# Performance work log

Measured on AMD Instinct MI355X. Metric: run time of the kernel, lower is better.

Reference implementation:

```python
import jax, jax.numpy as jnp
import numpy as np

HEADS = 16
DIM_HEAD = 64
DIM = 1024
INNER = HEADS * DIM_HEAD


def setup_inputs() -> dict:
    key = jax.random.key(0)
    k1, k2, k3, k4 = jax.random.split(key, 4)
    x = jax.random.normal(k1, (4, 2048, DIM), dtype=jnp.float32)
    W_qkv = jax.random.normal(k2, (DIM, 3 * INNER), dtype=jnp.float32) * (DIM ** -0.5)
    W_out = jax.random.normal(k3, (INNER, DIM), dtype=jnp.float32) * (INNER ** -0.5)
    b_out = jax.random.normal(k4, (DIM,), dtype=jnp.float32) * 0.01
    temperature = jnp.asarray(np.log(DIM_HEAD ** -0.5), dtype=jnp.float32)
    return {"x": x, "W_qkv": W_qkv, "W_out": W_out, "b_out": b_out,
            "temperature": temperature}


def reference(x, W_qkv, W_out, b_out, temperature):
    b, n, _ = x.shape
    qkv = jnp.einsum('bnd,de->bne', x, W_qkv)  # [b, n, 3*inner]
    q, k, v = jnp.split(qkv, 3, axis=-1)
    def split_heads(t):
        return t.reshape(b, n, HEADS, DIM_HEAD).transpose(0, 2, 1, 3)  # b h n d
    q, k, v = split_heads(q), split_heads(k), split_heads(v)
    scale = jnp.exp(temperature)
    dots = jnp.einsum('bhid,bhjd->bhij', q, k) * scale  # [b, h, n, n]
    mask_value = -jnp.finfo(dots.dtype).max
    eye = jnp.eye(n, dtype=bool)
    dots = jnp.where(eye, mask_value, dots)
    attn = jax.nn.softmax(dots, axis=-1)
    out = jnp.einsum('bhij,bhjd->bhid', attn, v)  # [b, h, n, d]
    out = out.transpose(0, 2, 1, 3).reshape(b, n, INNER)
    return jnp.einsum('bni,id->bnd', out, W_out) + b_out
```

## Files before the change

kernel.cpp:

```cpp
#include <hip/hip_runtime.h>


using u16 = unsigned short;
typedef short short8 __attribute__((ext_vector_type(8)));
typedef float floatx4 __attribute__((ext_vector_type(4)));
typedef float floatx16 __attribute__((ext_vector_type(16)));
typedef unsigned int uint2v __attribute__((ext_vector_type(2)));

#define B_ 4
#define N_ 2048
#define H_ 16
#define DH_ 64
#define D_ 1024
#define INNER_ 1024
#define M_ (B_ * N_)

__device__ __forceinline__ float bf2f(u16 h) {
    union { unsigned u; float f; } c; c.u = ((unsigned)h) << 16; return c.f;
}
__device__ __forceinline__ u16 f2bf(float f) {
    union { float f; unsigned u; } c; c.f = f;
    unsigned u = c.u + 0x7fffu + ((c.u >> 16) & 1u);
    return (u16)(u >> 16);
}
__device__ __forceinline__ unsigned cvtpk_bf16(float lo, float hi) {
    unsigned r;
    asm("v_cvt_pk_bf16_f32 %0, %1, %2" : "=v"(r) : "v"(lo), "v"(hi));
    return r;
}
__device__ __forceinline__ float fast_exp2(float x) {
#if defined(__has_builtin) && __has_builtin(__builtin_amdgcn_exp2f)
    return __builtin_amdgcn_exp2f(x);
#else
    return __expf(x * 0.69314718056f);
#endif
}
__device__ __forceinline__ void gl2lds16(const u16* g, u16* l) {
    __builtin_amdgcn_global_load_lds(
        (const __attribute__((address_space(1))) void*)g,
        (__attribute__((address_space(3))) void*)l, 16, 0, 0);
}

__global__ void detect_dtype(const u16* __restrict__ x, int* __restrict__ flag) {
    __shared__ int cnt;
    if (threadIdx.x == 0) cnt = 0;
    __syncthreads();
    int c = 0;
    for (int i = threadIdx.x; i < 4096; i += 256) {
        int e = (x[i] >> 7) & 0xFF;
        if (e >= 107 && e <= 147) c++;
    }
    atomicAdd(&cnt, c);
    __syncthreads();
    if (threadIdx.x == 0) flag[0] = (cnt >= 3584) ? 1 : 0;
}

__global__ __launch_bounds__(256) void convert_x(
    const void* __restrict__ in, u16* __restrict__ out, int n,
    const int* __restrict__ flag) {
    int f = flag[0];
    int i0 = (blockIdx.x * 256 + threadIdx.x) * 8;
    if (f) {
        const u16* p = (const u16*)in;
        for (int i = 0; i < 8; i++) out[i0 + i] = p[i0 + i];
    } else {
        const float* p = (const float*)in;
        for (int i = 0; i < 8; i++) out[i0 + i] = f2bf(p[i0 + i]);
    }
}

__global__ void prep_misc(const void* __restrict__ bias_in,
                          const void* __restrict__ temp_in,
                          float* __restrict__ bias_f, float* __restrict__ temp_f,
                          const int* __restrict__ flag) {
    int f = flag[0];
    for (int i = threadIdx.x; i < 1024; i += 256)
        bias_f[i] = f ? bf2f(((const u16*)bias_in)[i]) : ((const float*)bias_in)[i];
    if (threadIdx.x == 0)
        temp_f[0] = f ? bf2f(((const u16*)temp_in)[0]) : ((const float*)temp_in)[0];
}

__global__ __launch_bounds__(256) void transpose_cvt(
    const void* __restrict__ in, u16* __restrict__ out, int R, int C,
    const int* __restrict__ flag) {
    __shared__ u16 t[32][33];
    int f = flag[0];
    int tx = threadIdx.x & 31, ty = threadIdx.x >> 5;
    int c0 = blockIdx.x * 32, r0 = blockIdx.y * 32;
    for (int i = 0; i < 4; i++) {
        long idx = (long)(r0 + ty + i * 8) * C + c0 + tx;
        t[ty + i * 8][tx] = f ? ((const u16*)in)[idx] : f2bf(((const float*)in)[idx]);
    }
    __syncthreads();
    for (int i = 0; i < 4; i++)
        out[(long)(c0 + ty + i * 8) * R + r0 + tx] = t[tx][ty + i * 8];
}

__global__ __launch_bounds__(256) void transpose_v(
    const u16* __restrict__ in, u16* __restrict__ out) {
    __shared__ u16 t[32][33];
    const int bh = blockIdx.z;
    const u16* src = in + (long)bh * N_ * DH_;
    u16* dst = out + (long)bh * DH_ * N_;
    int tx = threadIdx.x & 31, ty = threadIdx.x >> 5;
    int r0 = blockIdx.y * 32;
    int c0 = blockIdx.x * 32;
    for (int i = 0; i < 4; i++)
        t[ty + i * 8][tx] = src[(long)(r0 + ty + i * 8) * DH_ + c0 + tx];
    __syncthreads();
    for (int i = 0; i < 4; i++)
        dst[(long)(c0 + ty + i * 8) * N_ + r0 + tx] = t[tx][ty + i * 8];
}

template <int MODE>
__global__ __launch_bounds__(256) void gemm_bt(
    const u16* __restrict__ A, const u16* __restrict__ Bt,
    int M, int N, int K,
    u16* __restrict__ out0, u16* __restrict__ out1, u16* __restrict__ out2,
    void* __restrict__ outv, const float* __restrict__ bias,
    const int* __restrict__ flag, const float* __restrict__ temp_f) {
    __shared__ __align__(16) u16 lA[128 * 32];
    __shared__ __align__(16) u16 lB[128 * 32];
    const int tid = threadIdx.x;
    const int lane = tid & 63;
    const int w = tid >> 6;
    const int wr = w >> 1, wc = w & 1;
    const int qd = lane >> 4, qm = lane & 15;
    const long m0 = (long)blockIdx.x * 128;
    const long n0 = (long)blockIdx.y * 128;

    floatx4 acc[4][4];
    for (int i = 0; i < 4; i++)
        for (int j = 0; j < 4; j++) acc[i][j] = (floatx4){0.f, 0.f, 0.f, 0.f};

    const int arow = lane >> 2;
    const int acol = ((lane & 3) ^ ((lane >> 3) & 3)) * 8;
    const int swz = (qm >> 1) & 3;

    for (int k0 = 0; k0 < K; k0 += 32) {
        for (int i = 0; i < 2; i++) {
            int c = w + i * 4;
            gl2lds16(A + (m0 + c * 16 + arow) * K + k0 + acol, lA + c * 512);
            gl2lds16(Bt + (n0 + c * 16 + arow) * K + k0 + acol, lB + c * 512);
        }
        __syncthreads();
        short8 af[4], bfr[4];
        for (int mt = 0; mt < 4; mt++)
            af[mt] = *(const short8*)&lA[(wr * 64 + mt * 16 + qm) * 32 + (qd ^ swz) * 8];
        for (int nt = 0; nt < 4; nt++)
            bfr[nt] = *(const short8*)&lB[(wc * 64 + nt * 16 + qm) * 32 + (qd ^ swz) * 8];
        for (int mt = 0; mt < 4; mt++)
            for (int nt = 0; nt < 4; nt++)
                acc[mt][nt] = __builtin_amdgcn_mfma_f32_16x16x32_bf16(
                    af[mt], bfr[nt], acc[mt][nt], 0, 0, 0);
        __syncthreads();
    }

    if (MODE == 0) {
        const float qscale = __expf(temp_f[0]) * 1.44269504089f;
        __shared__ __align__(16) u16 lC[64 * 132];
        for (int half = 0; half < 2; half++) {
            __syncthreads();
            if (wr == half) {
                for (int nt = 0; nt < 4; nt++) {
                    long ng = n0 + wc * 64 + nt * 16 + qm;
                    float sc = ((ng >> 10) == 0) ? qscale : 1.0f;
                    for (int mt = 0; mt < 4; mt++)
                        for (int r = 0; r < 4; r++)
                            lC[(mt * 16 + qd * 4 + r) * 132 + wc * 64 + nt * 16 + qm] =
                                f2bf(acc[mt][nt][r] * sc);
                }
            }
            __syncthreads();
            for (int i = 0; i < 4; i++) {
                int row = (tid >> 4) + i * 16;
                int c = (tid & 15) * 8;
                long m = m0 + half * 64 + row;
                long ngc = n0 + c;
                int part = (int)(ngc >> 10);
                int rem = (int)(ngc & 1023);
                int hh = rem >> 6, dh = rem & 63;
                long bb = m >> 11, n = m & 2047;
                long idx = ((bb * H_ + hh) * N_ + n) * DH_ + dh;
                short8 vv = *(const short8*)&lC[row * 132 + c];
                u16* dst = (part == 0) ? out0 : (part == 1) ? out1 : out2;
                *(short8*)&dst[idx] = vv;
            }
        }
    } else {
        const int f = flag[0];
        __shared__ __align__(16) float lCf[64 * 132];
        for (int half = 0; half < 2; half++) {
            __syncthreads();
            if (wr == half) {
                for (int nt = 0; nt < 4; nt++) {
                    long ng = n0 + wc * 64 + nt * 16 + qm;
                    float bv = bias[ng];
                    for (int mt = 0; mt < 4; mt++)
                        for (int r = 0; r < 4; r++)
                            lCf[(mt * 16 + qd * 4 + r) * 132 + wc * 64 + nt * 16 + qm] =
                                acc[mt][nt][r] + bv;
                }
            }
            __syncthreads();
            if (f) {
                for (int i = 0; i < 4; i++) {
                    int row = (tid >> 4) + i * 16;
                    int c = (tid & 15) * 8;
                    long m = m0 + half * 64 + row;
                    u16 tmp[8];
                    for (int j = 0; j < 8; j++) tmp[j] = f2bf(lCf[row * 132 + c + j]);
                    *(short8*)&((u16*)outv)[m * N + n0 + c] = *(const short8*)tmp;
                }
            } else {
                for (int i = 0; i < 8; i++) {
                    int row = (tid >> 5) + i * 8;
                    int c = (tid & 31) * 4;
                    long m = m0 + half * 64 + row;
                    floatx4 vv = *(const floatx4*)&lCf[row * 132 + c];
                    *(floatx4*)&((float*)outv)[m * N + n0 + c] = vv;
                }
            }
        }
    }
}

__global__ __launch_bounds__(256) void attn_kernel(
    const u16* __restrict__ q_ws, const u16* __restrict__ k_ws,
    const u16* __restrict__ vt_ws, u16* __restrict__ out) {
    __shared__ __align__(16) u16 lbuf[2 * 64 * 64];
    u16* lK = lbuf;
    u16* lV = lbuf + 64 * 64;
    const int tid = threadIdx.x, lane = tid & 63, w = tid >> 6;
    const int ln = lane & 31, h = lane >> 5;

    int linear = blockIdx.y * 16 + blockIdx.x;
    int bh = (linear & 7) * 8 + (linear >> 7);
    int q0 = ((linear >> 3) & 15) * 128;
    const int b = bh >> 4, hd = bh & 15;

    const u16* Q = q_ws + (long)bh * N_ * DH_;
    const u16* Kp = k_ws + (long)bh * N_ * DH_;
    const u16* Vt = vt_ws + (long)bh * DH_ * N_;

    const int qbase = q0 + w * 32;
    const int qrow = qbase + ln;

    short8 qa[4];
#pragma unroll
    for (int c = 0; c < 4; c++)
        qa[c] = *(const short8*)&Q[(long)qrow * DH_ + c * 16 + h * 8];

    floatx16 accO[2];
#pragma unroll
    for (int i = 0; i < 16; i++) { accO[0][i] = 0.f; accO[1][i] = 0.f; }
    float lacc = 0.f;

    const int srow = lane >> 3;
    const int scol = ((lane & 7) ^ srow) * 8;
    const int rsw = (ln & 7);

    for (int k0 = 0; k0 < N_; k0 += 64) {
        for (int i = 0; i < 2; i++) {
            int c = w + i * 4;
            gl2lds16(Kp + (long)(k0 + c * 8 + srow) * DH_ + scol, lK + c * 512);
            gl2lds16(Vt + (long)(c * 8 + srow) * N_ + k0 + scol, lV + c * 512);
        }
        __syncthreads();
        const bool diag = ((unsigned)(qbase - k0) < 64u);

#pragma unroll
        for (int kt = 0; kt < 2; kt++) {
            floatx16 accS;
#pragma unroll
            for (int i = 0; i < 16; i++) accS[i] = 0.f;
#pragma unroll
            for (int c = 0; c < 4; c++) {
                short8 kf = *(const short8*)
                    &lK[(kt * 32 + ln) * 64 + ((c * 2 + h) ^ rsw) * 8];
                accS = __builtin_amdgcn_mfma_f32_32x32x16_bf16(
                    kf, qa[c], accS, 0, 0, 0);
            }
            float rs = 0.f;
#pragma unroll
            for (int r = 0; r < 16; r++) {
                float pv = fast_exp2(accS[r]);
                if (diag) {
                    int key = k0 + kt * 32 + (r & 3) + 8 * (r >> 2) + 4 * h;
                    if (key == qrow) pv = 0.f;
                }
                accS[r] = pv;
                rs += pv;
            }
            lacc += rs;
#pragma unroll
            for (int ch = 0; ch < 2; ch++) {
                const int rb = ch * 8;
                unsigned d01 = cvtpk_bf16(accS[rb + 0], accS[rb + 1]);
                unsigned d23 = cvtpk_bf16(accS[rb + 2], accS[rb + 3]);
                unsigned d45 = cvtpk_bf16(accS[rb + 4], accS[rb + 5]);
                unsigned d67 = cvtpk_bf16(accS[rb + 6], accS[rb + 7]);
                uint2v s1 = __builtin_amdgcn_permlane32_swap(d01, d45, false, false);
                uint2v s2 = __builtin_amdgcn_permlane32_swap(d23, d67, false, false);
                union { unsigned u[4]; short8 v; } pf;
                pf.u[0] = s1[0]; pf.u[1] = s2[0]; pf.u[2] = s1[1]; pf.u[3] = s2[1];
                const int cc = kt * 2 + ch;
#pragma unroll
                for (int dt = 0; dt < 2; dt++) {
                    short8 vf = *(const short8*)
                        &lV[(dt * 32 + ln) * 64 + ((cc * 2 + h) ^ rsw) * 8];
                    accO[dt] = __builtin_amdgcn_mfma_f32_32x32x16_bf16(
                        vf, pf.v, accO[dt], 0, 0, 0);
                }
            }
        }
        __syncthreads();
    }

    lacc += __shfl_xor(lacc, 32, 64);
    const float inv = 1.f / lacc;

    u16* stg = (u16*)((char*)lbuf + w * 4096);
#pragma unroll
    for (int dt = 0; dt < 2; dt++)
#pragma unroll
        for (int q2 = 0; q2 < 4; q2++) {
            union { unsigned u[2]; unsigned long long ull; } ee;
            ee.u[0] = cvtpk_bf16(accO[dt][q2 * 4 + 0] * inv,
                                 accO[dt][q2 * 4 + 1] * inv);
            ee.u[1] = cvtpk_bf16(accO[dt][q2 * 4 + 2] * inv,
                                 accO[dt][q2 * 4 + 3] * inv);
            int G = dt * 4 + q2;
            *(unsigned long long*)
                &stg[ln * 64 + ((G ^ rsw) * 8) + h * 4] = ee.ull;
        }
    __syncthreads();
#pragma unroll
    for (int p = 0; p < 4; p++) {
        int R = p * 32 + (tid >> 3);
        int G = tid & 7;
        const u16* src = (const u16*)((char*)lbuf + (R >> 5) * 4096
                          + (R & 31) * 128 + ((G ^ (R & 7)) * 16));
        short8 vv = *(const short8*)src;
        *(short8*)&out[((long)(b * N_ + q0 + R)) * INNER_ + hd * DH_ + G * 8] = vv;
    }
}

extern "C" void kernel_launch(void* const* d_in, const int* in_sizes, int n_in,
                              void* d_out, int out_size, void* d_ws, size_t ws_size,
                              hipStream_t stream) {
    const void* x    = d_in[0];
    const void* Wqkv = d_in[1];
    const void* Wout = d_in[2];
    const void* bout = d_in[3];
    const void* temp = d_in[4];

    char* base = (char*)d_ws;
    int*   flag    = (int*)base;
    float* temp_f  = (float*)(base + 16);
    float* bias_f  = (float*)(base + 32);
    u16* xb      = (u16*)(base + 8192);
    u16* Wqkv_t  = xb + (long)M_ * D_;
    u16* Wout_t  = Wqkv_t + 3072 * 1024;
    u16* q_ws    = Wout_t + 1024 * 1024;
    u16* k_ws    = q_ws + (long)B_ * H_ * N_ * DH_;
    u16* vt_ws   = k_ws + (long)B_ * H_ * N_ * DH_;
    u16* attn_out = vt_ws + (long)B_ * H_ * N_ * DH_;
    u16* v_nat   = attn_out;

    dim3 blk(256);
    detect_dtype<<<1, blk, 0, stream>>>((const u16*)x, flag);
    convert_x<<<dim3(M_ * D_ / (256 * 8)), blk, 0, stream>>>(x, xb, M_ * D_, flag);
    prep_misc<<<1, blk, 0, stream>>>(bout, temp, bias_f, temp_f, flag);
    transpose_cvt<<<dim3(3 * INNER_ / 32, D_ / 32), blk, 0, stream>>>(
        Wqkv, Wqkv_t, D_, 3 * INNER_, flag);
    transpose_cvt<<<dim3(D_ / 32, INNER_ / 32), blk, 0, stream>>>(
        Wout, Wout_t, INNER_, D_, flag);
    gemm_bt<0><<<dim3(M_ / 128, 3 * INNER_ / 128), blk, 0, stream>>>(
        xb, Wqkv_t, M_, 3 * INNER_, D_, q_ws, k_ws, v_nat, nullptr, nullptr,
        flag, temp_f);
    transpose_v<<<dim3(DH_ / 32, N_ / 32, B_ * H_), blk, 0, stream>>>(
        v_nat, vt_ws);
    attn_kernel<<<dim3(N_ / 128, B_ * H_), blk, 0, stream>>>(
        q_ws, k_ws, vt_ws, attn_out);
    gemm_bt<1><<<dim3(M_ / 128, D_ / 128), blk, 0, stream>>>(
        attn_out, Wout_t, M_, D_, INNER_, nullptr, nullptr, nullptr, d_out,
        bias_f, flag, temp_f);
}
```

Measured before the change: 319.8 us.

## Double-buffer K/V tiles and process two query groups per wave in attention

The attention kernel now gives each block 256 queries, with each wave handling two 32-row query groups. Each K/V fragment loaded from LDS therefore feeds twice as many MFMAs. K/V tiles are double-buffered in LDS, so the next tile's global-to-LDS load is issued before the current tile is computed, and one barrier per iteration is removed. The cost is more registers per wave (two sets of accumulators and Q fragments), twice the LDS, and half as many blocks (512), which may lower occupancy and leave some CUs with unbalanced load.

```diff
diff --git a/kernel.cpp b/kernel.cpp
--- a/kernel.cpp
+++ b/kernel.cpp
@@ -228,118 +228,158 @@
 __global__ __launch_bounds__(256) void attn_kernel(
     const u16* __restrict__ q_ws, const u16* __restrict__ k_ws,
     const u16* __restrict__ vt_ws, u16* __restrict__ out) {
-    __shared__ __align__(16) u16 lbuf[2 * 64 * 64];
-    u16* lK = lbuf;
-    u16* lV = lbuf + 64 * 64;
+    __shared__ __align__(16) u16 lbuf[2 * 2 * 64 * 64];
     const int tid = threadIdx.x, lane = tid & 63, w = tid >> 6;
     const int ln = lane & 31, h = lane >> 5;
 
-    int linear = blockIdx.y * 16 + blockIdx.x;
-    int bh = (linear & 7) * 8 + (linear >> 7);
-    int q0 = ((linear >> 3) & 15) * 128;
+    int linear = blockIdx.y * 8 + blockIdx.x;
+    int bh = (linear & 7) * 8 + ((linear >> 6) & 7);
+    int q0 = ((linear >> 3) & 7) * 256;
     const int b = bh >> 4, hd = bh & 15;
 
     const u16* Q = q_ws + (long)bh * N_ * DH_;
     const u16* Kp = k_ws + (long)bh * N_ * DH_;
     const u16* Vt = vt_ws + (long)bh * DH_ * N_;
 
-    const int qbase = q0 + w * 32;
-    const int qrow = qbase + ln;
-
-    short8 qa[4];
-#pragma unroll
-    for (int c = 0; c < 4; c++)
-        qa[c] = *(const short8*)&Q[(long)qrow * DH_ + c * 16 + h * 8];
-
-    floatx16 accO[2];
-#pragma unroll
-    for (int i = 0; i < 16; i++) { accO[0][i] = 0.f; accO[1][i] = 0.f; }
-    float lacc = 0.f;
+    const int qbase = q0 + w * 64;
+
+    short8 qa[2][4];
+#pragma unroll
+    for (int g = 0; g < 2; g++)
+#pragma unroll
+        for (int c = 0; c < 4; c++)
+            qa[g][c] = *(const short8*)
+                &Q[(long)(qbase + g * 32 + ln) * DH_ + c * 16 + h * 8];
+
+    floatx16 accO[2][2];
+#pragma unroll
+    for (int i = 0; i < 16; i++) {
+        accO[0][0][i] = 0.f; accO[0][1][i] = 0.f;
+        accO[1][0][i] = 0.f; accO[1][1][i] = 0.f;
+    }
+    float lacc[2] = {0.f, 0.f};
 
     const int srow = lane >> 3;
     const int scol = ((lane & 7) ^ srow) * 8;
     const int rsw = (ln & 7);
 
-    for (int k0 = 0; k0 < N_; k0 += 64) {
+    {
+        u16* nK = lbuf;
+        u16* nV = lbuf + 4096;
         for (int i = 0; i < 2; i++) {
             int c = w + i * 4;
-            gl2lds16(Kp + (long)(k0 + c * 8 + srow) * DH_ + scol, lK + c * 512);
-            gl2lds16(Vt + (long)(c * 8 + srow) * N_ + k0 + scol, lV + c * 512);
-        }
-        __syncthreads();
-        const bool diag = ((unsigned)(qbase - k0) < 64u);
+            gl2lds16(Kp + (long)(c * 8 + srow) * DH_ + scol, nK + c * 512);
+            gl2lds16(Vt + (long)(c * 8 + srow) * N_ + scol, nV + c * 512);
+        }
+    }
+    __syncthreads();
+
+    for (int t = 0; t < 32; t++) {
+        const int k0 = t * 64;
+        const u16* lK = lbuf + (t & 1) * 8192;
+        const u16* lV = lK + 4096;
+        if (t < 31) {
+            u16* nK = lbuf + ((t + 1) & 1) * 8192;
+            u16* nV = nK + 4096;
+            for (int i = 0; i < 2; i++) {
+                int c = w + i * 4;
+                gl2lds16(Kp + (long)(k0 + 64 + c * 8 + srow) * DH_ + scol,
+                         nK + c * 512);
+                gl2lds16(Vt + (long)(c * 8 + srow) * N_ + k0 + 64 + scol,
+                         nV + c * 512);
+            }
+        }
 
 #pragma unroll
         for (int kt = 0; kt < 2; kt++) {
-            floatx16 accS;
-#pragma unroll
-            for (int i = 0; i < 16; i++) accS[i] = 0.f;
+            floatx16 accS[2];
+#pragma unroll
+            for (int i = 0; i < 16; i++) { accS[0][i] = 0.f; accS[1][i] = 0.f; }
 #pragma unroll
             for (int c = 0; c < 4; c++) {
                 short8 kf = *(const short8*)
                     &lK[(kt * 32 + ln) * 64 + ((c * 2 + h) ^ rsw) * 8];
-                accS = __builtin_amdgcn_mfma_f32_32x32x16_bf16(
-                    kf, qa[c], accS, 0, 0, 0);
-            }
-            float rs = 0.f;
-#pragma unroll
-            for (int r = 0; r < 16; r++) {
-                float pv = fast_exp2(accS[r]);
-                if (diag) {
-                    int key = k0 + kt * 32 + (r & 3) + 8 * (r >> 2) + 4 * h;
-                    if (key == qrow) pv = 0.f;
-                }
-                accS[r] = pv;
-                rs += pv;
-            }
-            lacc += rs;
+                accS[0] = __builtin_amdgcn_mfma_f32_32x32x16_bf16(
+                    kf, qa[0][c], accS[0], 0, 0, 0);
+                accS[1] = __builtin_amdgcn_mfma_f32_32x32x16_bf16(
+                    kf, qa[1][c], accS[1], 0, 0, 0);
+            }
+#pragma unroll
+            for (int g = 0; g < 2; g++) {
+#pragma unroll
+                for (int r = 0; r < 16; r++)
+                    accS[g][r] = fast_exp2(accS[g][r]);
+                if ((qbase + g * 32) == (k0 + kt * 32)) {
+#pragma unroll
+                    for (int r = 0; r < 16; r++) {
+                        int kk = (r & 3) + 8 * (r >> 2) + 4 * h;
+                        if (kk == ln) accS[g][r] = 0.f;
+                    }
+                }
+                float rs = (((accS[g][0] + accS[g][1]) + (accS[g][2] + accS[g][3]))
+                          + ((accS[g][4] + accS[g][5]) + (accS[g][6] + accS[g][7])))
+                         + (((accS[g][8] + accS[g][9]) + (accS[g][10] + accS[g][11]))
+                          + ((accS[g][12] + accS[g][13]) + (accS[g][14] + accS[g][15])));
+                lacc[g] += rs;
+            }
 #pragma unroll
             for (int ch = 0; ch < 2; ch++) {
                 const int rb = ch * 8;
-                unsigned d01 = cvtpk_bf16(accS[rb + 0], accS[rb + 1]);
-                unsigned d23 = cvtpk_bf16(accS[rb + 2], accS[rb + 3]);
-                unsigned d45 = cvtpk_bf16(accS[rb + 4], accS[rb + 5]);
-                unsigned d67 = cvtpk_bf16(accS[rb + 6], accS[rb + 7]);
-                uint2v s1 = __builtin_amdgcn_permlane32_swap(d01, d45, false, false);
-                uint2v s2 = __builtin_amdgcn_permlane32_swap(d23, d67, false, false);
-                union { unsigned u[4]; short8 v; } pf;
-                pf.u[0] = s1[0]; pf.u[1] = s2[0]; pf.u[2] = s1[1]; pf.u[3] = s2[1];
+                short8 pfv[2];
+#pragma unroll
+                for (int g = 0; g < 2; g++) {
+                    unsigned d01 = cvtpk_bf16(accS[g][rb + 0], accS[g][rb + 1]);
+                    unsigned d23 = cvtpk_bf16(accS[g][rb + 2], accS[g][rb + 3]);
+                    unsigned d45 = cvtpk_bf16(accS[g][rb + 4], accS[g][rb + 5]);
+                    unsigned d67 = cvtpk_bf16(accS[g][rb + 6], accS[g][rb + 7]);
+                    uint2v s1 = __builtin_amdgcn_permlane32_swap(d01, d45, false, false);
+                    uint2v s2 = __builtin_amdgcn_permlane32_swap(d23, d67, false, false);
+                    union { unsigned u[4]; short8 v; } pf;
+                    pf.u[0] = s1[0]; pf.u[1] = s2[0]; pf.u[2] = s1[1]; pf.u[3] = s2[1];
+                    pfv[g] = pf.v;
+                }
                 const int cc = kt * 2 + ch;
 #pragma unroll
                 for (int dt = 0; dt < 2; dt++) {
                     short8 vf = *(const short8*)
                         &lV[(dt * 32 + ln) * 64 + ((cc * 2 + h) ^ rsw) * 8];
-                    accO[dt] = __builtin_amdgcn_mfma_f32_32x32x16_bf16(
-                        vf, pf.v, accO[dt], 0, 0, 0);
+                    accO[0][dt] = __builtin_amdgcn_mfma_f32_32x32x16_bf16(
+                        vf, pfv[0], accO[0][dt], 0, 0, 0);
+                    accO[1][dt] = __builtin_amdgcn_mfma_f32_32x32x16_bf16(
+                        vf, pfv[1], accO[1][dt], 0, 0, 0);
                 }
             }
         }
         __syncthreads();
     }
 
-    lacc += __shfl_xor(lacc, 32, 64);
-    const float inv = 1.f / lacc;
-
-    u16* stg = (u16*)((char*)lbuf + w * 4096);
-#pragma unroll
-    for (int dt = 0; dt < 2; dt++)
-#pragma unroll
-        for (int q2 = 0; q2 < 4; q2++) {
-            union { unsigned u[2]; unsigned long long ull; } ee;
-            ee.u[0] = cvtpk_bf16(accO[dt][q2 * 4 + 0] * inv,
-                                 accO[dt][q2 * 4 + 1] * inv);
-            ee.u[1] = cvtpk_bf16(accO[dt][q2 * 4 + 2] * inv,
-                                 accO[dt][q2 * 4 + 3] * inv);
-            int G = dt * 4 + q2;
-            *(unsigned long long*)
-                &stg[ln * 64 + ((G ^ rsw) * 8) + h * 4] = ee.ull;
-        }
-    __syncthreads();
-#pragma unroll
-    for (int p = 0; p < 4; p++) {
+#pragma unroll
+    for (int g = 0; g < 2; g++) {
+        float s = lacc[g];
+        s += __shfl_xor(s, 32, 64);
+        const float inv = 1.f / s;
+        u16* stg = (u16*)((char*)lbuf + w * 8192 + g * 4096);
+#pragma unroll
+        for (int dt = 0; dt < 2; dt++)
+#pragma unroll
+            for (int q2 = 0; q2 < 4; q2++) {
+                union { unsigned u[2]; unsigned long long ull; } ee;
+                ee.u[0] = cvtpk_bf16(accO[g][dt][q2 * 4 + 0] * inv,
+                                     accO[g][dt][q2 * 4 + 1] * inv);
+                ee.u[1] = cvtpk_bf16(accO[g][dt][q2 * 4 + 2] * inv,
+                                     accO[g][dt][q2 * 4 + 3] * inv);
+                int G = dt * 4 + q2;
+                *(unsigned long long*)
+                    &stg[ln * 64 + ((G ^ rsw) * 8) + h * 4] = ee.ull;
+            }
+    }
+    __syncthreads();
+#pragma unroll
+    for (int p = 0; p < 8; p++) {
         int R = p * 32 + (tid >> 3);
         int G = tid & 7;
-        const u16* src = (const u16*)((char*)lbuf + (R >> 5) * 4096
+        const u16* src = (const u16*)((char*)lbuf + (R >> 6) * 8192
+                          + ((R >> 5) & 1) * 4096
                           + (R & 31) * 128 + ((G ^ (R & 7)) * 16));
         short8 vv = *(const short8*)src;
         *(short8*)&out[((long)(b * N_ + q0 + R)) * INNER_ + hd * DH_ + G * 8] = vv;
@@ -381,7 +421,7 @@
         flag, temp_f);
     transpose_v<<<dim3(DH_ / 32, N_ / 32, B_ * H_), blk, 0, stream>>>(
         v_nat, vt_ws);
-    attn_kernel<<<dim3(N_ / 128, B_ * H_), blk, 0, stream>>>(
+    attn_kernel<<<dim3(N_ / 256, B_ * H_), blk, 0, stream>>>(
         q_ws, k_ws, vt_ws, attn_out);
     gemm_bt<1><<<dim3(M_ / 128, D_ / 128), blk, 0, stream>>>(
         attn_out, Wout_t, M_, D_, INNER_, nullptr, nullptr, nullptr, d_out,
```

After: 302.7 us. -5.3%, faster.
